# Optimization experiments

Hardware: AMD Instinct MI355X
Metric: run time of the kernel (lower is better)

The kernel has to match this reference:

```python
import jax, jax.numpy as jnp
import numpy as np

N = 50000          # nodes
E = 1600000        # edges
H = 8              # heads
F = 16             # out feats per head (np1class)
IN = 256           # in feats
NEG_SLOPE = 0.2    # DGL GATConv default leaky_relu slope


def setup_inputs() -> dict:
    key = jax.random.key(0)
    ks = jax.random.split(key, 7)
    x = jax.random.normal(ks[0], (N, IN), dtype=jnp.float32)
    W = jax.random.normal(ks[1], (IN, H * F), dtype=jnp.float32) * 0.05
    attn_l = jax.random.normal(ks[2], (H, F), dtype=jnp.float32) * 0.05
    attn_r = jax.random.normal(ks[3], (H, F), dtype=jnp.float32) * 0.05
    bias = jax.random.normal(ks[4], (H * F,), dtype=jnp.float32) * 0.05
    src = jax.random.randint(ks[5], (E,), 0, N, dtype=jnp.int64)
    dst = jax.random.randint(ks[6], (E,), 0, N, dtype=jnp.int64)
    return {"x": x, "W": W, "attn_l": attn_l, "attn_r": attn_r,
            "bias": bias, "src": src, "dst": dst}


def reference(x, W, attn_l, attn_r, bias, src, dst):
    # Linear projection to heads: [N, H, F]
    feat = (x @ W).reshape(N, H, F)
    # Per-node attention halves: [N, H]
    el = jnp.einsum('nhf,hf->nh', feat, attn_l)
    er = jnp.einsum('nhf,hf->nh', feat, attn_r)
    # Edge scores: e = leaky_relu(el[src] + er[dst])  -> [E, H]
    e = jax.nn.leaky_relu(el[src] + er[dst], negative_slope=NEG_SLOPE)
    # Segment softmax over incoming edges of each destination node
    m = jax.ops.segment_max(e, dst, num_segments=N)           # [N, H]
    m = jnp.where(jnp.isfinite(m), m, 0.0)                    # empty segments
    m = jax.lax.stop_gradient(m)
    ex = jnp.exp(e - m[dst])                                  # [E, H]
    s = jax.ops.segment_sum(ex, dst, num_segments=N)          # [N, H]
    a = ex / jnp.maximum(s[dst], 1e-9)                        # [E, H]
    # Weighted aggregation of source features: [N, H, F]
    msg = a[:, :, None] * feat[src]
    rst = jax.ops.segment_sum(msg, dst, num_segments=N)
    rst = rst + bias.reshape(H, F)
    # Classifier: mean over heads -> [N, F]
    return rst.mean(axis=1)
```

## Files before the change

### kernel.cpp

```cpp
#include <hip/hip_runtime.h>
#include <hip/hip_bf16.h>

#define NH 8
#define NF 16
#define NIN 256
#define HF 128
#define CAP 3072
#define BCH 4096

typedef __attribute__((ext_vector_type(8))) short bf16x8;
typedef __attribute__((ext_vector_type(4))) float f32x4;

__device__ __forceinline__ unsigned short f2bf(float f) {
    union { float f; unsigned int u; } v; v.f = f;
    unsigned int r = v.u + 0x7FFFu + ((v.u >> 16) & 1u);
    return (unsigned short)(r >> 16);
}
__device__ __forceinline__ float bf2f(unsigned short b) {
    union { unsigned int u; float f; } v; v.u = ((unsigned int)b) << 16;
    return v.f;
}

#define GROWS 128
__global__ __launch_bounds__(256) void gemm_mfma(const float* __restrict__ A,
                                                 const float* __restrict__ W,
                                                 const float* __restrict__ attn_l,
                                                 const float* __restrict__ attn_r,
                                                 unsigned short* __restrict__ featb,
                                                 float* __restrict__ el,
                                                 float* __restrict__ er, int M) {
    __shared__ unsigned short AsH[32][264];
    __shared__ unsigned short AsL[32][264];
    const int tid = threadIdx.x;
    const int wave = tid >> 6, lane = tid & 63;
    const int quad = lane >> 4, lq = lane & 15;
    const int row0 = blockIdx.x * GROWS;

    bf16x8 bfrag[8][2];
#pragma unroll
    for (int h2 = 0; h2 < 2; h2++) {
        const int col = (wave * 2 + h2) * 16 + lq;
#pragma unroll
        for (int kk = 0; kk < 8; kk++) {
            const int kb = kk * 32 + quad * 8;
            bf16x8 f;
#pragma unroll
            for (int j = 0; j < 8; j++)
                f[j] = (short)f2bf(W[(size_t)(kb + j) * HF + col]);
            bfrag[kk][h2] = f;
        }
    }
    const float al0 = attn_l[(wave * 2 + 0) * 16 + lq];
    const float al1 = attn_l[(wave * 2 + 1) * 16 + lq];
    const float ar0 = attn_r[(wave * 2 + 0) * 16 + lq];
    const float ar1 = attn_r[(wave * 2 + 1) * 16 + lq];

    const int srow = tid >> 3;

    for (int c = 0; c < 4; c++) {
        const int crow0 = row0 + c * 32;
        __syncthreads();
#pragma unroll
        for (int i = 0; i < 8; i++) {
            const int col = ((tid & 7) + i * 8) * 4;
            const int gr = crow0 + srow;
            float4 v = make_float4(0.f, 0.f, 0.f, 0.f);
            if (gr < M) v = *(const float4*)&A[(size_t)gr * NIN + col];
            const unsigned short h0 = f2bf(v.x), h1 = f2bf(v.y),
                                 h2b = f2bf(v.z), h3 = f2bf(v.w);
            *(ushort4*)&AsH[srow][col] = make_ushort4(h0, h1, h2b, h3);
            *(ushort4*)&AsL[srow][col] =
                make_ushort4(f2bf(v.x - bf2f(h0)), f2bf(v.y - bf2f(h1)),
                             f2bf(v.z - bf2f(h2b)), f2bf(v.w - bf2f(h3)));
        }
        __syncthreads();
#pragma unroll
        for (int s = 0; s < 2; s++) {
            f32x4 acc0 = {0.f, 0.f, 0.f, 0.f};
            f32x4 acc1 = {0.f, 0.f, 0.f, 0.f};
            const int ar = s * 16 + lq;
#pragma unroll
            for (int kk = 0; kk < 8; kk++) {
                const bf16x8 ah = *(const bf16x8*)&AsH[ar][kk * 32 + quad * 8];
                const bf16x8 al = *(const bf16x8*)&AsL[ar][kk * 32 + quad * 8];
                acc0 = __builtin_amdgcn_mfma_f32_16x16x32_bf16(ah, bfrag[kk][0], acc0, 0, 0, 0);
                acc1 = __builtin_amdgcn_mfma_f32_16x16x32_bf16(ah, bfrag[kk][1], acc1, 0, 0, 0);
                acc0 = __builtin_amdgcn_mfma_f32_16x16x32_bf16(al, bfrag[kk][0], acc0, 0, 0, 0);
                acc1 = __builtin_amdgcn_mfma_f32_16x16x32_bf16(al, bfrag[kk][1], acc1, 0, 0, 0);
            }
#pragma unroll
            for (int r = 0; r < 4; r++) {
                const int gr = crow0 + s * 16 + quad * 4 + r;
                float pl0 = acc0[r] * al0, pr0 = acc0[r] * ar0;
                float pl1 = acc1[r] * al1, pr1 = acc1[r] * ar1;
#pragma unroll
                for (int m = 1; m < 16; m <<= 1) {
                    pl0 += __shfl_xor(pl0, m, 64);
                    pr0 += __shfl_xor(pr0, m, 64);
                    pl1 += __shfl_xor(pl1, m, 64);
                    pr1 += __shfl_xor(pr1, m, 64);
                }
                if (gr < M) {
                    featb[(size_t)gr * HF + (wave * 2 + 0) * 16 + lq] = f2bf(acc0[r]);
                    featb[(size_t)gr * HF + (wave * 2 + 1) * 16 + lq] = f2bf(acc1[r]);
                    if (lq == 0) {
                        el[(size_t)gr * NH + wave * 2 + 0] = pl0;
                        el[(size_t)gr * NH + wave * 2 + 1] = pl1;
                        er[(size_t)gr * NH + wave * 2 + 0] = pr0;
                        er[(size_t)gr * NH + wave * 2 + 1] = pr1;
                    }
                }
            }
        }
    }
}

__global__ __launch_bounds__(256) void bin_kernel(const int* __restrict__ src,
                                                  const int* __restrict__ dst,
                                                  int* __restrict__ bcnt,
                                                  unsigned int* __restrict__ binned,
                                                  int E, int NB) {
    __shared__ unsigned int hist[800];
    __shared__ unsigned short lpos[BCH];
    __shared__ int dcache[BCH];
    const int tid = threadIdx.x;
    const int base = blockIdx.x * BCH;
    const int cnt = min(BCH, E - base);
    for (int b = tid; b < NB; b += 256) hist[b] = 0;
    for (int i = tid; i < cnt; i += 256) dcache[i] = dst[base + i];
    __syncthreads();
    for (int i = tid; i < cnt; i += 256)
        lpos[i] = (unsigned short)atomicAdd(&hist[dcache[i] >> 6], 1u);
    __syncthreads();
    for (int b = tid; b < NB; b += 256) {
        const unsigned int c = hist[b];
        if (c) hist[b] = (unsigned int)(b * CAP + atomicAdd(&bcnt[b], (int)c));
    }
    __syncthreads();
    for (int i = tid; i < cnt; i += 256) {
        const int d = dcache[i];
        const int b = d >> 6;
        binned[hist[b] + (unsigned int)lpos[i]] =
            (unsigned int)src[base + i] | ((unsigned int)(d & 63) << 16);
    }
}

__global__ __launch_bounds__(256) void csr_kernel(const int* __restrict__ bcnt,
                                                  const unsigned int* __restrict__ binned,
                                                  int* __restrict__ nodeinfo,
                                                  unsigned short* __restrict__ srcsw,
                                                  int N) {
    __shared__ int len[64], cur[64];
    const int b = blockIdx.x, t = threadIdx.x;
    const int node0 = b << 6;
    const int cntb = bcnt[b];
    const unsigned int* bb = &binned[(size_t)b * CAP];
    unsigned short* sw = &srcsw[(size_t)b * CAP];
    if (t < 64) len[t] = 0;
    __syncthreads();
    for (int i = t; i < cntb; i += 256) atomicAdd(&len[bb[i] >> 16], 1);
    __syncthreads();
    if (t < 64) {
        const int v = len[t];
        int incl = v;
#pragma unroll
        for (int off = 1; off < 64; off <<= 1) {
            const int x = __shfl_up(incl, off, 64);
            if (t >= off) incl += x;
        }
        const int excl = incl - v;
        cur[t] = excl;
        if (node0 + t < N) nodeinfo[node0 + t] = excl | (v << 16);
    }
    __syncthreads();
    for (int i = t; i < cntb; i += 256) {
        const unsigned int p = bb[i];
        const int pos = atomicAdd(&cur[p >> 16], 1);
        sw[pos] = (unsigned short)(p & 0xFFFFu);
    }
}

__global__ __launch_bounds__(128) void agg_kernel(const int* __restrict__ nodeinfo,
                                                  const unsigned short* __restrict__ srcsw,
                                                  const float* __restrict__ el,
                                                  const float* __restrict__ er,
                                                  const unsigned short* __restrict__ featb,
                                                  const float* __restrict__ bias,
                                                  float* __restrict__ out) {
    const int n = blockIdx.x;
    const int tid = threadIdx.x;
    __shared__ float lds_sc[32][8];
    __shared__ int lds_src[32];
    __shared__ float lds_ps[128];
    __shared__ float lds_s[8];
    __shared__ float2 lds_acc[2][64];
    __shared__ float2 lds_v[8][8];

    const int info = nodeinfo[n];
    const int begin = (n >> 6) * CAP + (info & 0xFFFF);
    const int end = begin + (info >> 16);
    const int hA = tid & 7, eA = tid >> 3;
    const float er_h = er[(size_t)n * NH + hA];
    const int w = tid >> 6, lane = tid & 63;
    const int hB = lane >> 3, fB2 = lane & 7;

    float2 acc = make_float2(0.f, 0.f);
    float psum = 0.f;
    for (int base = begin; base < end; base += 32) {
        const int cn = min(32, end - base);
#pragma unroll
        for (int rep = 0; rep < 2; rep++) {
            const int ei = eA + rep * 16;
            if (ei < cn) {
                const int si = (int)srcsw[base + ei];
                if (hA == 0) lds_src[ei] = si;
                float v = el[(size_t)si * NH + hA] + er_h;
                v = v > 0.f ? v : 0.2f * v;
                const float sc = __expf(v);
                lds_sc[ei][hA] = sc;
                psum += sc;
            }
        }
        __syncthreads();
        unsigned int fv[16];
#pragma unroll
        for (int j = 0; j < 16; j++) {
            const int ej = w * 16 + j;
            const int sj = lds_src[ej];
            fv[j] = (ej < cn)
                        ? *(const unsigned int*)&featb[(size_t)sj * HF + hB * 16 + fB2 * 2]
                        : 0u;
        }
#pragma unroll
        for (int j = 0; j < 16; j++) {
            const int ej = w * 16 + j;
            const float sc = (ej < cn) ? lds_sc[ej][hB] : 0.f;
            acc.x = fmaf(sc, bf2f((unsigned short)(fv[j] & 0xFFFFu)), acc.x);
            acc.y = fmaf(sc, bf2f((unsigned short)(fv[j] >> 16)), acc.y);
        }
        __syncthreads();
    }

    lds_ps[tid] = psum;
    lds_acc[w][lane] = acc;
    __syncthreads();
    if (tid < 8) {
        float s = 0.f;
#pragma unroll
        for (int k = 0; k < 16; k++) s += lds_ps[k * 8 + tid];
        lds_s[tid] = fmaxf(s, 1e-9f);
    }
    __syncthreads();
    if (tid < 64) {
        const float2 t0 = lds_acc[0][tid], t1 = lds_acc[1][tid];
        const float inv = 1.f / lds_s[hB];
        float2 val;
        val.x = (t0.x + t1.x) * inv + bias[hB * 16 + fB2 * 2];
        val.y = (t0.y + t1.y) * inv + bias[hB * 16 + fB2 * 2 + 1];
        lds_v[hB][fB2] = val;
    }
    __syncthreads();
    if (tid < 8) {
        float2 o = make_float2(0.f, 0.f);
#pragma unroll
        for (int h = 0; h < 8; h++) {
            const float2 v = lds_v[h][tid];
            o.x += v.x; o.y += v.y;
        }
        o.x *= 0.125f; o.y *= 0.125f;
        *(float2*)&out[(size_t)n * 16 + tid * 2] = o;
    }
}

extern "C" void kernel_launch(void* const* d_in, const int* in_sizes, int n_in,
                              void* d_out, int out_size, void* d_ws, size_t ws_size,
                              hipStream_t stream) {
    const float* x      = (const float*)d_in[0];
    const float* W      = (const float*)d_in[1];
    const float* attn_l = (const float*)d_in[2];
    const float* attn_r = (const float*)d_in[3];
    const float* bias   = (const float*)d_in[4];
    const int*   src    = (const int*)d_in[5];
    const int*   dst    = (const int*)d_in[6];
    float* out = (float*)d_out;

    const int N = in_sizes[0] / NIN;
    const int E = in_sizes[5];
    const int NB = (N + 63) >> 6;

    char* w = (char*)d_ws;
    unsigned short* featb = (unsigned short*)w; w += (size_t)N * HF * 2;
    float* el     = (float*)w; w += (size_t)N * NH * 4;
    float* er     = (float*)w; w += (size_t)N * NH * 4;
    int* nodeinfo = (int*)w;   w += (size_t)N * 4;
    int* bcnt     = (int*)w;   w += (size_t)((NB + 15) & ~15) * 4;
    unsigned int* binned = (unsigned int*)w; w += (size_t)NB * CAP * 4;
    unsigned short* srcsw = (unsigned short*)w;

    hipMemsetAsync(bcnt, 0, (size_t)NB * sizeof(int), stream);

    gemm_mfma<<<(N + GROWS - 1) / GROWS, 256, 0, stream>>>(x, W, attn_l, attn_r,
                                                           featb, el, er, N);
    bin_kernel<<<(E + BCH - 1) / BCH, 256, 0, stream>>>(src, dst, bcnt, binned, E, NB);
    csr_kernel<<<NB, 256, 0, stream>>>(bcnt, binned, nodeinfo, srcsw, N);
    agg_kernel<<<N, 128, 0, stream>>>(nodeinfo, srcsw, el, er, featb, bias, out);
}
```

Measured before the change: 243.4 us.

## Replace atomic global binning with per-block local sort plus run-offset table

The edge binning now sorts each 4096-edge chunk locally in LDS and writes it contiguously, recording per-chunk bucket run offsets and counts in a table instead of using global atomics to scatter edges into fixed-capacity buckets. A new prefix kernel walks the table serially per bucket to compute where each chunk's run lands, and the CSR kernel gathers runs from all chunks into LDS before building the per-node lists and writing them out coalesced. This aims to remove global atomic contention and scattered writes and to drop the memset, at the cost of an extra launch, a serial loop over about 391 chunks per bucket, and many small uncoalesced reads in the CSR gather.

```diff
diff --git a/kernel.cpp b/kernel.cpp
--- a/kernel.cpp
+++ b/kernel.cpp
@@ -117,48 +117,99 @@
 
 __global__ __launch_bounds__(256) void bin_kernel(const int* __restrict__ src,
                                                   const int* __restrict__ dst,
-                                                  int* __restrict__ bcnt,
                                                   unsigned int* __restrict__ binned,
+                                                  unsigned int* __restrict__ runtab,
                                                   int E, int NB) {
-    __shared__ unsigned int hist[800];
+    __shared__ unsigned int hist[784];
+    __shared__ unsigned int offs[784];
     __shared__ unsigned short lpos[BCH];
+    __shared__ unsigned int obuf[BCH];
     __shared__ int dcache[BCH];
-    const int tid = threadIdx.x;
-    const int base = blockIdx.x * BCH;
+    __shared__ unsigned int wsum[4];
+    __shared__ unsigned int sbase;
+    const int blk = blockIdx.x, t = threadIdx.x;
+    const int base = blk * BCH;
     const int cnt = min(BCH, E - base);
-    for (int b = tid; b < NB; b += 256) hist[b] = 0;
-    for (int i = tid; i < cnt; i += 256) dcache[i] = dst[base + i];
-    __syncthreads();
-    for (int i = tid; i < cnt; i += 256)
+    const int lane = t & 63, w = t >> 6;
+    for (int b = t; b < NB; b += 256) hist[b] = 0;
+    for (int i = t; i < cnt; i += 256) dcache[i] = dst[base + i];
+    if (t == 0) sbase = 0;
+    __syncthreads();
+    for (int i = t; i < cnt; i += 256)
         lpos[i] = (unsigned short)atomicAdd(&hist[dcache[i] >> 6], 1u);
     __syncthreads();
-    for (int b = tid; b < NB; b += 256) {
-        const unsigned int c = hist[b];
-        if (c) hist[b] = (unsigned int)(b * CAP + atomicAdd(&bcnt[b], (int)c));
-    }
-    __syncthreads();
-    for (int i = tid; i < cnt; i += 256) {
+    for (int c0 = 0; c0 < NB; c0 += 256) {
+        const int idx = c0 + t;
+        const unsigned int v = (idx < NB) ? hist[idx] : 0;
+        unsigned int incl = v;
+#pragma unroll
+        for (int off = 1; off < 64; off <<= 1) {
+            const unsigned int x = __shfl_up(incl, off, 64);
+            if (lane >= off) incl += x;
+        }
+        if (lane == 63) wsum[w] = incl;
+        __syncthreads();
+        unsigned int wbase = 0;
+        for (int k = 0; k < w; k++) wbase += wsum[k];
+        const unsigned int tot = wsum[0] + wsum[1] + wsum[2] + wsum[3];
+        const unsigned int excl = sbase + wbase + incl - v;
+        if (idx < NB) {
+            offs[idx] = excl;
+            runtab[(size_t)blk * NB + idx] = excl | (v << 16);
+        }
+        __syncthreads();
+        if (t == 0) sbase += tot;
+        __syncthreads();
+    }
+    for (int i = t; i < cnt; i += 256) {
         const int d = dcache[i];
-        const int b = d >> 6;
-        binned[hist[b] + (unsigned int)lpos[i]] =
+        obuf[offs[d >> 6] + lpos[i]] =
             (unsigned int)src[base + i] | ((unsigned int)(d & 63) << 16);
     }
-}
-
-__global__ __launch_bounds__(256) void csr_kernel(const int* __restrict__ bcnt,
-                                                  const unsigned int* __restrict__ binned,
+    __syncthreads();
+    for (int i = t; i < cnt; i += 256) binned[(size_t)base + i] = obuf[i];
+}
+
+__global__ __launch_bounds__(256) void prefix_kernel(const unsigned int* __restrict__ runtab,
+                                                     unsigned int* __restrict__ combo,
+                                                     int NB, int nbb) {
+    const int b = blockIdx.x * 256 + threadIdx.x;
+    if (b >= NB) return;
+    unsigned int acc = 0;
+    unsigned int* cb = &combo[(size_t)b * (nbb + 1)];
+    for (int blk = 0; blk < nbb; blk++) {
+        const unsigned int e = runtab[(size_t)blk * NB + b];
+        cb[blk] = (e & 0xFFFu) | (acc << 12);
+        acc += (e >> 16);
+    }
+    cb[nbb] = (acc << 12);
+}
+
+__global__ __launch_bounds__(256) void csr_kernel(const unsigned int* __restrict__ binned,
+                                                  const unsigned int* __restrict__ combo,
                                                   int* __restrict__ nodeinfo,
                                                   unsigned short* __restrict__ srcsw,
-                                                  int N) {
+                                                  int N, int nbb) {
+    __shared__ unsigned int eary[CAP];
+    __shared__ unsigned short sSrc[CAP];
     __shared__ int len[64], cur[64];
+    __shared__ int tot_s;
     const int b = blockIdx.x, t = threadIdx.x;
     const int node0 = b << 6;
-    const int cntb = bcnt[b];
-    const unsigned int* bb = &binned[(size_t)b * CAP];
-    unsigned short* sw = &srcsw[(size_t)b * CAP];
+    const unsigned int* cb = &combo[(size_t)b * (nbb + 1)];
+    for (int r = t; r < nbb; r += 256) {
+        const unsigned int c0 = cb[r], c1 = cb[r + 1];
+        const int off = (int)(c0 & 0xFFFu);
+        const int pb = (int)(c0 >> 12);
+        const int rc = (int)(c1 >> 12) - pb;
+        const unsigned int* bp = &binned[(size_t)r * BCH + off];
+        for (int j = 0; j < rc; j++) eary[pb + j] = bp[j];
+    }
     if (t < 64) len[t] = 0;
-    __syncthreads();
-    for (int i = t; i < cntb; i += 256) atomicAdd(&len[bb[i] >> 16], 1);
+    if (t == 0) tot_s = (int)(cb[nbb] >> 12);
+    __syncthreads();
+    const int tot = tot_s;
+    for (int i = t; i < tot; i += 256) atomicAdd(&len[eary[i] >> 16], 1);
     __syncthreads();
     if (t < 64) {
         const int v = len[t];
@@ -173,11 +224,14 @@
         if (node0 + t < N) nodeinfo[node0 + t] = excl | (v << 16);
     }
     __syncthreads();
-    for (int i = t; i < cntb; i += 256) {
-        const unsigned int p = bb[i];
+    for (int i = t; i < tot; i += 256) {
+        const unsigned int p = eary[i];
         const int pos = atomicAdd(&cur[p >> 16], 1);
-        sw[pos] = (unsigned short)(p & 0xFFFFu);
-    }
+        sSrc[pos] = (unsigned short)(p & 0xFFFFu);
+    }
+    __syncthreads();
+    unsigned short* sw = &srcsw[(size_t)b * CAP];
+    for (int i = t; i < tot; i += 256) sw[i] = sSrc[i];
 }
 
 __global__ __launch_bounds__(128) void agg_kernel(const int* __restrict__ nodeinfo,
@@ -287,21 +341,22 @@
     const int N = in_sizes[0] / NIN;
     const int E = in_sizes[5];
     const int NB = (N + 63) >> 6;
+    const int nbb = (E + BCH - 1) / BCH;
 
     char* w = (char*)d_ws;
     unsigned short* featb = (unsigned short*)w; w += (size_t)N * HF * 2;
     float* el     = (float*)w; w += (size_t)N * NH * 4;
     float* er     = (float*)w; w += (size_t)N * NH * 4;
     int* nodeinfo = (int*)w;   w += (size_t)N * 4;
-    int* bcnt     = (int*)w;   w += (size_t)((NB + 15) & ~15) * 4;
-    unsigned int* binned = (unsigned int*)w; w += (size_t)NB * CAP * 4;
+    unsigned int* binned = (unsigned int*)w; w += (size_t)nbb * BCH * 4;
+    unsigned int* runtab = (unsigned int*)w; w += (size_t)nbb * NB * 4;
+    unsigned int* combo  = (unsigned int*)w; w += (size_t)NB * (nbb + 1) * 4;
     unsigned short* srcsw = (unsigned short*)w;
-
-    hipMemsetAsync(bcnt, 0, (size_t)NB * sizeof(int), stream);
 
     gemm_mfma<<<(N + GROWS - 1) / GROWS, 256, 0, stream>>>(x, W, attn_l, attn_r,
                                                            featb, el, er, N);
-    bin_kernel<<<(E + BCH - 1) / BCH, 256, 0, stream>>>(src, dst, bcnt, binned, E, NB);
-    csr_kernel<<<NB, 256, 0, stream>>>(bcnt, binned, nodeinfo, srcsw, N);
+    bin_kernel<<<nbb, 256, 0, stream>>>(src, dst, binned, runtab, E, NB);
+    prefix_kernel<<<(NB + 255) / 256, 256, 0, stream>>>(runtab, combo, NB, nbb);
+    csr_kernel<<<NB, 256, 0, stream>>>(binned, combo, nodeinfo, srcsw, N, nbb);
     agg_kernel<<<N, 128, 0, stream>>>(nodeinfo, srcsw, el, er, featb, bias, out);
 }
```

Result: slower. 359.5 us (+47.7%).
